# Performance work log

Hardware: AMD Instinct MI355X
Metric: run time of the kernel (lower is better)

Reference implementation:

```python
import jax, jax.numpy as jnp
import numpy as np

POOL = 7  # fixed 7x7 output grid, hard-coded in the original layer


def _bin_bounds(step, rlen):
    # Replicates the original bin-corner logic + empty-bin adjustment.
    i = jnp.arange(POOL, dtype=jnp.int32)
    s = i * step
    e = jnp.where(i < POOL - 1, (i + 1) * step, rlen)
    empty = s == e
    # original: grow end by 1 if room, else shrink start by 1
    e = jnp.where(empty & (e < rlen), e + 1, e)
    s = jnp.where(empty & ~(e > (i * step)) , s, s)  # no-op placeholder for clarity
    s = jnp.where(empty & ((i * step) == e), (i * step) - 1, jnp.where(empty, i * step, s))
    # simpler equivalent: if still empty after trying to grow end, shrink start
    s0 = i * step
    e0 = jnp.where(i < POOL - 1, (i + 1) * step, rlen)
    grow = empty & (e0 < rlen)
    e = jnp.where(grow, e0 + 1, e0)
    s = jnp.where(empty & ~grow, s0 - 1, s0)
    return s, e


def _pool_one(roi, fm):
    # fm: [H, W, C]; roi: [4] normalized (y1, x1, y2, x2)
    H, W, C = fm.shape
    h0 = (H * roi[0]).astype(jnp.int32)  # tf.cast to int32 truncates (floor for >=0)
    w0 = (W * roi[1]).astype(jnp.int32)
    h1 = (H * roi[2]).astype(jnp.int32)
    w1 = (W * roi[3]).astype(jnp.int32)
    rh = h1 - h0
    rw = w1 - w0
    hstep = rh // POOL
    wstep = rw // POOL
    sh, eh = _bin_bounds(hstep, rh)  # [7], region-relative
    sw, ew = _bin_bounds(wstep, rw)
    hidx = jnp.arange(H, dtype=jnp.int32)
    widx = jnp.arange(W, dtype=jnp.int32)
    rmask = (hidx[None, :] >= (h0 + sh)[:, None]) & (hidx[None, :] < (h0 + eh)[:, None])  # [7,H]
    cmask = (widx[None, :] >= (w0 + sw)[:, None]) & (widx[None, :] < (w0 + ew)[:, None])  # [7,W]
    neg = jnp.asarray(-jnp.inf, fm.dtype)
    # max over rows for each of the 7 row-bins: [7, W, C]
    t = jnp.max(jnp.where(rmask[:, :, None, None], fm[None, :, :, :], neg), axis=1)
    # max over cols for each of the 7 col-bins: [7, 7, C]
    out = jnp.max(jnp.where(cmask[None, :, :, None], t[:, None, :, :], neg), axis=2)
    return out


def setup_inputs() -> dict:
    key = jax.random.key(0)
    k_f, k_y, k_x, k_h, k_w = jax.random.split(key, 5)
    H, W, C, N = 50, 50, 1024, 300
    features = jax.random.normal(k_f, (1, H, W, C), dtype=jnp.float32)
    # well-formed normalized ROIs: y1 < y2, x1 < x2, extent in [0.2, 0.55]
    y1 = jax.random.uniform(k_y, (N,), minval=0.0, maxval=0.45)
    x1 = jax.random.uniform(k_x, (N,), minval=0.0, maxval=0.45)
    hh = jax.random.uniform(k_h, (N,), minval=0.2, maxval=0.55)
    ww = jax.random.uniform(k_w, (N,), minval=0.2, maxval=0.55)
    rois = jnp.stack([y1, x1, jnp.minimum(y1 + hh, 1.0), jnp.minimum(x1 + ww, 1.0)], axis=1).astype(jnp.float32)
    return {"features": features, "rois": rois}


def reference(features, rois):
    fm = jnp.squeeze(features, axis=0)  # [H, W, C]
    # sequential over ROIs (mirrors tf.while_loop), fully vectorized per ROI
    pooled = jax.lax.map(lambda r: _pool_one(r, fm), rois)  # [N, 7, 7, C]
    return pooled
```

## Files before the change

kernel.cpp:

```cpp
#include <hip/hip_runtime.h>
#include <math.h>

#define POOL 7
#define FH 50
#define FW 50
#define FC 1024
#define FC4 (FC / 4)
#define CHUNKS 4
#define F4C 64
#define ROWSTRIDE (FW * FC4)
#define JGROUPS 4
#define UNITS_PER_ROI (POOL * JGROUPS)

typedef float vf4 __attribute__((ext_vector_type(4)));

static __device__ __forceinline__ vf4 vmax4(vf4 a, vf4 b) {
    vf4 r;
    r.x = fmaxf(a.x, b.x);
    r.y = fmaxf(a.y, b.y);
    r.z = fmaxf(a.z, b.z);
    r.w = fmaxf(a.w, b.w);
    return r;
}

__global__ __launch_bounds__(256) void roipool_kernel(
    const float* __restrict__ fm,
    const float* __restrict__ rois,
    float* __restrict__ out,
    int nunits)
{
    const int b     = blockIdx.x;
    const int chunk = b & (CHUNKS - 1);
    const int wave  = threadIdx.x >> 6;
    const int lane  = threadIdx.x & 63;
    const int u     = (b >> 2) * 4 + wave;
    if (u >= nunits) return;

    const int n   = u / UNITS_PER_ROI;
    const int rem = u - n * UNITS_PER_ROI;
    const int i   = rem >> 2;
    const int jg  = rem & 3;
    const int j0  = jg * 2;
    const int jcnt = (jg < JGROUPS - 1) ? 2 : 1;

    const float4 roi = reinterpret_cast<const float4*>(rois)[n];
    const int h0 = (int)((float)FH * roi.x);
    const int w0 = (int)((float)FW * roi.y);
    const int h1 = (int)((float)FH * roi.z);
    const int w1 = (int)((float)FW * roi.w);
    const int rh = h1 - h0;
    const int rw = w1 - w0;
    const int hstep = rh / POOL;
    const int wstep = rw / POOL;

    int sh = i * hstep;
    int eh = (i < POOL - 1) ? (i + 1) * hstep : rh;
    if (sh == eh) { if (eh < rh) eh += 1; else sh -= 1; }
    const int r0 = max(0, h0 + sh);
    const int r1 = min(FH, h0 + eh);

    int c0[2], c1[2];
#pragma unroll
    for (int t = 0; t < 2; ++t) {
        const int j = j0 + t;
        if (j < POOL) {
            int sw = j * wstep;
            int ew = (j < POOL - 1) ? (j + 1) * wstep : rw;
            if (sw == ew) { if (ew < rw) ew += 1; else sw -= 1; }
            c0[t] = max(0, w0 + sw);
            c1[t] = min(FW, w0 + ew);
        } else {
            c0[t] = 0; c1[t] = 0;
        }
    }

    const int f4 = chunk * F4C + lane;
    const vf4* fmbase = reinterpret_cast<const vf4*>(fm) + f4;

    vf4 acc[2];
#pragma unroll
    for (int t = 0; t < 2; ++t) {
        acc[t].x = -INFINITY; acc[t].y = -INFINITY;
        acc[t].z = -INFINITY; acc[t].w = -INFINITY;
    }

    for (int r = r0; r < r1; ++r) {
        const vf4* rowp = fmbase + r * ROWSTRIDE;
#pragma unroll
        for (int t = 0; t < 2; ++t) {
            int c = c0[t];
            const int ce = c1[t];
            for (; c + 1 < ce; c += 2) {
                vf4 a  = rowp[c * FC4];
                vf4 b2 = rowp[(c + 1) * FC4];
                acc[t] = vmax4(acc[t], vmax4(a, b2));
            }
            if (c < ce) {
                acc[t] = vmax4(acc[t], rowp[c * FC4]);
            }
        }
    }

    vf4* o = reinterpret_cast<vf4*>(out) + (size_t)(n * 49 + i * 7 + j0) * FC4 + f4;
    __builtin_nontemporal_store(acc[0], o);
    if (jcnt == 2) {
        __builtin_nontemporal_store(acc[1], o + (size_t)FC4);
    }
}

extern "C" void kernel_launch(void* const* d_in, const int* in_sizes, int n_in,
                              void* d_out, int out_size, void* d_ws, size_t ws_size,
                              hipStream_t stream) {
    const float* features = (const float*)d_in[0];
    const float* rois     = (const float*)d_in[1];
    float* out            = (float*)d_out;
    const int N = in_sizes[1] / 4;

    const int nunits = N * UNITS_PER_ROI;
    dim3 grid(((nunits + 3) / 4) * CHUNKS);
    dim3 block(256);
    roipool_kernel<<<grid, block, 0, stream>>>(features, rois, out, nunits);
}
```

Baseline: 98.60 us.

## Transpose feature map into chunk-major slabs before ROI pooling

Adds a pre-pass that copies the feature map into a workspace laid out so each 256-channel chunk forms its own contiguous slab over all cells. The pooling kernel is templated on strides and reads from this layout, so each chunk's working set is compact (about 2.5 MB) and should cache better. The cost is an extra kernel launch plus a full copy of the 10 MB feature map on every call, and it falls back to the original path if the workspace is too small.

```diff
diff --git a/kernel.cpp b/kernel.cpp
--- a/kernel.cpp
+++ b/kernel.cpp
@@ -8,7 +8,8 @@
 #define FC4 (FC / 4)
 #define CHUNKS 4
 #define F4C 64
-#define ROWSTRIDE (FW * FC4)
+#define NCELLS (FH * FW)
+#define CHSLAB (NCELLS * F4C)
 #define JGROUPS 4
 #define UNITS_PER_ROI (POOL * JGROUPS)
 
@@ -23,8 +24,22 @@
     return r;
 }
 
+__global__ __launch_bounds__(256) void chunkmajor_kernel(
+    const float* __restrict__ fm,
+    float* __restrict__ fmT)
+{
+    const int b     = blockIdx.x;
+    const int chunk = b & (CHUNKS - 1);
+    const int cg    = b >> 2;
+    const int cell  = cg * 4 + (threadIdx.x >> 6);
+    const int lane  = threadIdx.x & 63;
+    const vf4 v = reinterpret_cast<const vf4*>(fm)[(size_t)cell * FC4 + chunk * F4C + lane];
+    reinterpret_cast<vf4*>(fmT)[(size_t)chunk * CHSLAB + (size_t)cell * F4C + lane] = v;
+}
+
+template<int CSTRIDE, int CHSTRIDE>
 __global__ __launch_bounds__(256) void roipool_kernel(
-    const float* __restrict__ fm,
+    const float* __restrict__ src,
     const float* __restrict__ rois,
     float* __restrict__ out,
     int nunits)
@@ -74,8 +89,9 @@
         }
     }
 
-    const int f4 = chunk * F4C + lane;
-    const vf4* fmbase = reinterpret_cast<const vf4*>(fm) + f4;
+    const int rowstride = FW * CSTRIDE;
+    const vf4* base = reinterpret_cast<const vf4*>(src)
+                    + (size_t)chunk * CHSTRIDE + lane;
 
     vf4 acc[2];
 #pragma unroll
@@ -85,23 +101,24 @@
     }
 
     for (int r = r0; r < r1; ++r) {
-        const vf4* rowp = fmbase + r * ROWSTRIDE;
+        const vf4* rowp = base + (size_t)r * rowstride;
 #pragma unroll
         for (int t = 0; t < 2; ++t) {
             int c = c0[t];
             const int ce = c1[t];
             for (; c + 1 < ce; c += 2) {
-                vf4 a  = rowp[c * FC4];
-                vf4 b2 = rowp[(c + 1) * FC4];
+                vf4 a  = rowp[c * CSTRIDE];
+                vf4 b2 = rowp[(c + 1) * CSTRIDE];
                 acc[t] = vmax4(acc[t], vmax4(a, b2));
             }
             if (c < ce) {
-                acc[t] = vmax4(acc[t], rowp[c * FC4]);
+                acc[t] = vmax4(acc[t], rowp[c * CSTRIDE]);
             }
         }
     }
 
-    vf4* o = reinterpret_cast<vf4*>(out) + (size_t)(n * 49 + i * 7 + j0) * FC4 + f4;
+    const int of4 = chunk * F4C + lane;
+    vf4* o = reinterpret_cast<vf4*>(out) + (size_t)(n * 49 + i * 7 + j0) * FC4 + of4;
     __builtin_nontemporal_store(acc[0], o);
     if (jcnt == 2) {
         __builtin_nontemporal_store(acc[1], o + (size_t)FC4);
@@ -119,5 +136,13 @@
     const int nunits = N * UNITS_PER_ROI;
     dim3 grid(((nunits + 3) / 4) * CHUNKS);
     dim3 block(256);
-    roipool_kernel<<<grid, block, 0, stream>>>(features, rois, out, nunits);
+
+    const size_t needT = (size_t)CHUNKS * CHSLAB * 4 * sizeof(float);
+    if (ws_size >= needT) {
+        float* fmT = (float*)d_ws;
+        chunkmajor_kernel<<<dim3((NCELLS / 4) * CHUNKS), block, 0, stream>>>(features, fmT);
+        roipool_kernel<F4C, CHSLAB><<<grid, block, 0, stream>>>(fmT, rois, out, nunits);
+    } else {
+        roipool_kernel<FC4, F4C><<<grid, block, 0, stream>>>(features, rois, out, nunits);
+    }
 }
```

Result: slower. 101.5 us (+2.9%).

## Precompute 2x2 max-pooled feature map and split bins across half-waves

Applied to the files above, without the earlier changes.

Adds a pre-pass kernel that builds a 2x2 sliding-window max of the feature map in workspace, so each bin reads about a quarter as many vectors by covering it with overlapping clamped 2x2 windows. The main kernel now uses a fixed persistent grid with a grid-stride loop over units. Each wave is split into two halves that cover alternating columns and are combined with a cross-lane shuffle. This cuts global loads per bin at the cost of an extra launch, a full feature-map read and write, and shuffle overhead.

```diff
diff --git a/kernel.cpp b/kernel.cpp
--- a/kernel.cpp
+++ b/kernel.cpp
@@ -6,11 +6,13 @@
 #define FW 50
 #define FC 1024
 #define FC4 (FC / 4)
-#define CHUNKS 4
-#define F4C 64
-#define ROWSTRIDE (FW * FC4)
+#define CHUNKS 8
+#define F4C 32
 #define JGROUPS 4
 #define UNITS_PER_ROI (POOL * JGROUPS)
+#define GRID 2048
+#define NCELLS (FH * FW)
+#define QBYTES ((size_t)NCELLS * FC * sizeof(float))
 
 typedef float vf4 __attribute__((ext_vector_type(4)));
 
@@ -23,88 +25,144 @@
     return r;
 }
 
-__global__ __launch_bounds__(256) void roipool_kernel(
+__global__ __launch_bounds__(256) void build_q(
+    const float* __restrict__ fm, float* __restrict__ q)
+{
+    const int cell = blockIdx.x;
+    const int t    = threadIdx.x;
+    const int r    = cell / FW;
+    const int c    = cell - r * FW;
+    const int r1   = (r + 1 < FH) ? r + 1 : r;
+    const int c1   = (c + 1 < FW) ? c + 1 : c;
+    const vf4* f = reinterpret_cast<const vf4*>(fm);
+    const vf4 v = vmax4(
+        vmax4(f[(size_t)(r  * FW + c ) * FC4 + t], f[(size_t)(r1 * FW + c ) * FC4 + t]),
+        vmax4(f[(size_t)(r  * FW + c1) * FC4 + t], f[(size_t)(r1 * FW + c1) * FC4 + t]));
+    reinterpret_cast<vf4*>(q)[(size_t)cell * FC4 + t] = v;
+}
+
+static __device__ __forceinline__ void do_bin(
+    const vf4* __restrict__ qbase, const vf4* __restrict__ fbase, int haveQ,
+    int r0, int hr, int colb, int wc, int half, vf4& acc)
+{
+    if (haveQ && hr >= 2 && wc >= 2) {
+        const int rmax = r0 + hr - 2;
+        const int cmax = colb + wc - 2;
+        const int RP = (hr + 1) >> 1;
+        const int KQ = (wc + 3) >> 2;
+        for (int rp = 0; rp < RP; ++rp) {
+            const int qr = min(r0 + 2 * rp, rmax);
+            const vf4* rowp = qbase + (size_t)(qr * FW) * F4C * (FC4 / F4C);
+            for (int k = 0; k < KQ; ++k) {
+                const int qa = min(colb + 4 * k + 2 * half, cmax);
+                acc = vmax4(acc, rowp[(size_t)qa * FC4]);
+            }
+        }
+    } else {
+        const int clast = colb + wc - 1;
+        const int KP = (wc + 1) >> 1;
+        for (int r = r0; r < r0 + hr; ++r) {
+            const vf4* rowp = fbase + (size_t)(r * FW) * FC4;
+            for (int k = 0; k < KP; ++k) {
+                const int ca = min(colb + 2 * k + half, clast);
+                acc = vmax4(acc, rowp[(size_t)ca * FC4]);
+            }
+        }
+    }
+}
+
+static __device__ __forceinline__ vf4 cross_half_max(vf4 a) {
+    vf4 o;
+    o.x = __shfl_xor(a.x, 32, 64);
+    o.y = __shfl_xor(a.y, 32, 64);
+    o.z = __shfl_xor(a.z, 32, 64);
+    o.w = __shfl_xor(a.w, 32, 64);
+    return vmax4(a, o);
+}
+
+__global__ __launch_bounds__(256, 4) void roipool_kernel(
     const float* __restrict__ fm,
     const float* __restrict__ rois,
     float* __restrict__ out,
-    int nunits)
+    int nunits,
+    const float* __restrict__ q, int haveQ)
 {
     const int b     = blockIdx.x;
     const int chunk = b & (CHUNKS - 1);
     const int wave  = threadIdx.x >> 6;
     const int lane  = threadIdx.x & 63;
-    const int u     = (b >> 2) * 4 + wave;
-    if (u >= nunits) return;
+    const int half  = lane >> 5;
+    const int sl    = lane & 31;
+    const int wv    = (b >> 3) * 4 + wave;
 
-    const int n   = u / UNITS_PER_ROI;
-    const int rem = u - n * UNITS_PER_ROI;
-    const int i   = rem >> 2;
-    const int jg  = rem & 3;
-    const int j0  = jg * 2;
-    const int jcnt = (jg < JGROUPS - 1) ? 2 : 1;
+    const int f4 = chunk * F4C + sl;
+    const vf4* fbase = reinterpret_cast<const vf4*>(fm) + f4;
+    const vf4* qbase = reinterpret_cast<const vf4*>(q) + f4;
 
-    const float4 roi = reinterpret_cast<const float4*>(rois)[n];
-    const int h0 = (int)((float)FH * roi.x);
-    const int w0 = (int)((float)FW * roi.y);
-    const int h1 = (int)((float)FH * roi.z);
-    const int w1 = (int)((float)FW * roi.w);
-    const int rh = h1 - h0;
-    const int rw = w1 - w0;
-    const int hstep = rh / POOL;
-    const int wstep = rw / POOL;
+    for (int u = wv; u < nunits; u += 1024) {
+        const int n   = u / UNITS_PER_ROI;
+        const int rem = u - n * UNITS_PER_ROI;
+        const int i   = rem >> 2;
+        const int jg  = rem & 3;
+        const int j0  = jg * 2;
+        const int jcnt = (jg < JGROUPS - 1) ? 2 : 1;
 
-    int sh = i * hstep;
-    int eh = (i < POOL - 1) ? (i + 1) * hstep : rh;
-    if (sh == eh) { if (eh < rh) eh += 1; else sh -= 1; }
-    const int r0 = max(0, h0 + sh);
-    const int r1 = min(FH, h0 + eh);
+        const float4 roi = reinterpret_cast<const float4*>(rois)[n];
+        const int h0 = (int)((float)FH * roi.x);
+        const int w0 = (int)((float)FW * roi.y);
+        const int h1 = (int)((float)FH * roi.z);
+        const int w1 = (int)((float)FW * roi.w);
+        const int rh = h1 - h0;
+        const int rw = w1 - w0;
+        const int hstep = rh / POOL;
+        const int wstep = rw / POOL;
 
-    int c0[2], c1[2];
-#pragma unroll
-    for (int t = 0; t < 2; ++t) {
-        const int j = j0 + t;
-        if (j < POOL) {
-            int sw = j * wstep;
-            int ew = (j < POOL - 1) ? (j + 1) * wstep : rw;
-            if (sw == ew) { if (ew < rw) ew += 1; else sw -= 1; }
-            c0[t] = max(0, w0 + sw);
-            c1[t] = min(FW, w0 + ew);
+        vf4* o = reinterpret_cast<vf4*>(out)
+               + (size_t)(n * 49 + i * 7 + j0) * FC4 + f4;
+
+        if (hstep >= 1 && wstep >= 1) {
+            const int r0 = h0 + i * hstep;
+            const int hr = (i < POOL - 1) ? hstep : (rh - 6 * hstep);
+            {
+                const int wc   = (jg < 3) ? wstep : (rw - 6 * wstep);
+                const int colb = w0 + j0 * wstep;
+                vf4 a = {-INFINITY, -INFINITY, -INFINITY, -INFINITY};
+                do_bin(qbase, fbase, haveQ, r0, hr, colb, wc, half, a);
+                a = cross_half_max(a);
+                if (half == 0) __builtin_nontemporal_store(a, o);
+            }
+            if (jcnt == 2) {
+                const int colb = w0 + (j0 + 1) * wstep;
+                vf4 a = {-INFINITY, -INFINITY, -INFINITY, -INFINITY};
+                do_bin(qbase, fbase, haveQ, r0, hr, colb, wstep, half, a);
+                a = cross_half_max(a);
+                if (half == 0) __builtin_nontemporal_store(a, o + (size_t)FC4);
+            }
         } else {
-            c0[t] = 0; c1[t] = 0;
-        }
-    }
+            int sh = i * hstep;
+            int eh = (i < POOL - 1) ? (i + 1) * hstep : rh;
+            if (sh == eh) { if (eh < rh) eh += 1; else sh -= 1; }
+            const int rr0 = max(0, h0 + sh);
+            const int rr1 = min(FH, h0 + eh);
 
-    const int f4 = chunk * F4C + lane;
-    const vf4* fmbase = reinterpret_cast<const vf4*>(fm) + f4;
-
-    vf4 acc[2];
-#pragma unroll
-    for (int t = 0; t < 2; ++t) {
-        acc[t].x = -INFINITY; acc[t].y = -INFINITY;
-        acc[t].z = -INFINITY; acc[t].w = -INFINITY;
-    }
-
-    for (int r = r0; r < r1; ++r) {
-        const vf4* rowp = fmbase + r * ROWSTRIDE;
-#pragma unroll
-        for (int t = 0; t < 2; ++t) {
-            int c = c0[t];
-            const int ce = c1[t];
-            for (; c + 1 < ce; c += 2) {
-                vf4 a  = rowp[c * FC4];
-                vf4 b2 = rowp[(c + 1) * FC4];
-                acc[t] = vmax4(acc[t], vmax4(a, b2));
-            }
-            if (c < ce) {
-                acc[t] = vmax4(acc[t], rowp[c * FC4]);
+            for (int t = 0; t < jcnt; ++t) {
+                const int j = j0 + t;
+                int sw = j * wstep;
+                int ew = (j < POOL - 1) ? (j + 1) * wstep : rw;
+                if (sw == ew) { if (ew < rw) ew += 1; else sw -= 1; }
+                const int cc0 = max(0, w0 + sw);
+                const int cc1 = min(FW, w0 + ew);
+                vf4 a = {-INFINITY, -INFINITY, -INFINITY, -INFINITY};
+                if (cc1 > cc0 && rr1 > rr0) {
+                    do_bin(qbase, fbase, 0, rr0, rr1 - rr0, cc0, cc1 - cc0,
+                           half, a);
+                }
+                a = cross_half_max(a);
+                if (half == 0) {
+                    __builtin_nontemporal_store(a, o + (size_t)t * FC4);
+                }
             }
         }
-    }
-
-    vf4* o = reinterpret_cast<vf4*>(out) + (size_t)(n * 49 + i * 7 + j0) * FC4 + f4;
-    __builtin_nontemporal_store(acc[0], o);
-    if (jcnt == 2) {
-        __builtin_nontemporal_store(acc[1], o + (size_t)FC4);
     }
 }
 
@@ -115,9 +173,16 @@
     const float* rois     = (const float*)d_in[1];
     float* out            = (float*)d_out;
     const int N = in_sizes[1] / 4;
+    const int nunits = N * UNITS_PER_ROI;
 
-    const int nunits = N * UNITS_PER_ROI;
-    dim3 grid(((nunits + 3) / 4) * CHUNKS);
     dim3 block(256);
-    roipool_kernel<<<grid, block, 0, stream>>>(features, rois, out, nunits);
+    int haveQ = 0;
+    float* qptr = nullptr;
+    if (ws_size >= QBYTES) {
+        qptr = (float*)d_ws;
+        haveQ = 1;
+        build_q<<<dim3(NCELLS), block, 0, stream>>>(features, qptr);
+    }
+    roipool_kernel<<<dim3(GRID), block, 0, stream>>>(features, rois, out,
+                                                     nunits, qptr, haveQ);
 }
```

After: 106.2 us. +7.7%, slower.
